# Kernel tuning notes

Measured on AMD Instinct MI355X. Metric: run time of the kernel, lower is better.

The kernel has to match this reference:

```python
import jax, jax.numpy as jnp
import numpy as np

C, H, W = 8, 8, 8
A = 6            # action_dim
LATENT = 64
HID = 64
GRU_IN = HID + A + LATENT  # 134


def _conv(x, w):
    return jax.lax.conv_general_dilated(
        x, w, (1, 1), 'VALID', dimension_numbers=('NCHW', 'OIHW', 'NCHW'))


def setup_inputs() -> dict:
    key = jax.random.key(0)
    ks = jax.random.split(key, 20)
    B, N, T = 64, 10, 128
    s_h = jax.random.normal(ks[0], (B, N, T, C, H, W), jnp.float32)
    a_h = jax.random.randint(ks[1], (B, N, T), 0, A).astype(jnp.int64)
    b_z = jax.random.normal(ks[2], (B, LATENT), jnp.float32)
    s = 0.05
    p = {
        'conv1_w': jax.random.normal(ks[3], (32, C, 3, 3)) * s,
        'conv1_b': jnp.zeros((32,)),
        'conv2_w': jax.random.normal(ks[4], (32, 32, 3, 3)) * s,
        'conv2_b': jnp.zeros((32,)),
        'fc_w': jax.random.normal(ks[5], (HID, 32 * 4 * 4)) * s,
        'fc_b': jnp.zeros((HID,)),
        'emb': jax.random.normal(ks[6], (A, A)) * s,
        'gru_wih': jax.random.normal(ks[7], (3 * HID, GRU_IN)) * s,
        'gru_whh': jax.random.normal(ks[8], (3 * HID, HID)) * s,
        'gru_bih': jnp.zeros((3 * HID,)),
        'gru_bhh': jnp.zeros((3 * HID,)),
        'mlp1_w': jax.random.normal(ks[9], (HID, HID)) * s,
        'mlp1_b': jnp.zeros((HID,)),
        'mlp2_w': jax.random.normal(ks[10], (A, HID)) * s,
        'mlp2_b': jnp.zeros((A,)),
    }
    return {'s_h': s_h, 'a_h': a_h, 'b_z': b_z, **p}


def reference(s_h, a_h, b_z, conv1_w, conv1_b, conv2_w, conv2_b, fc_w, fc_b,
              emb, gru_wih, gru_whh, gru_bih, gru_bhh,
              mlp1_w, mlp1_b, mlp2_w, mlp2_b):
    B, N = s_h.shape[0], s_h.shape[1]
    T = a_h.shape[2]
    BN = B * N

    # action mask, [B, N, T, 1]
    action_masks = (a_h != A - 1)[..., None].astype(jnp.float32)

    # --- state encoder on first frame only ---
    s0 = s_h[:, :, 0].reshape(BN, C, H, W)
    x = jax.nn.relu(_conv(s0, conv1_w) + conv1_b[:, None, None])
    x = jax.nn.relu(_conv(x, conv2_w) + conv2_b[:, None, None])
    x = x.reshape(BN, -1)                       # [BN, 512]
    state_emb = jax.nn.relu(x @ fc_w.T + fc_b)  # [BN, HID]

    bz = jnp.broadcast_to(b_z[:, None, :], (B, N, LATENT)).reshape(BN, LATENT)

    h0 = jnp.zeros((BN, HID), s_h.dtype)
    act0 = jnp.full((BN,), A - 1, jnp.int32)

    def step(carry, _):
        h, act = carry
        a_emb = emb[act]                                          # [BN, A]
        inp = jnp.concatenate([state_emb, a_emb, bz], axis=-1)    # [BN, GRU_IN]
        gx = inp @ gru_wih.T + gru_bih
        gh = h @ gru_whh.T + gru_bhh
        xr, xz, xn = jnp.split(gx, 3, axis=-1)
        hr, hz, hn = jnp.split(gh, 3, axis=-1)
        r = jax.nn.sigmoid(xr + hr)
        z = jax.nn.sigmoid(xz + hz)
        n = jnp.tanh(xn + r * hn)
        h_new = (1.0 - z) * n + z * h
        hid = jnp.tanh(h_new @ mlp1_w.T + mlp1_b)
        logits = hid @ mlp2_w.T + mlp2_b                          # [BN, A]
        next_act = jax.lax.stop_gradient(jnp.argmax(logits, axis=-1)).astype(jnp.int32)
        return (h_new, next_act), logits

    (_, _), logits_seq = jax.lax.scan(step, (h0, act0), None, length=T - 1)
    # logits_seq: [T-1, BN, A] -> [B, N, T-1, A]
    logits_all = jnp.transpose(logits_seq, (1, 0, 2)).reshape(B, N, T - 1, A)
    return logits_all, action_masks
```

## Files before the change

### kernel.cpp

```cpp
#include <hip/hip_runtime.h>

#define A_DIM 6
#define HID_D 64
#define LATENT_D 64
#define GRU_IN_D 134
#define T_STEPS 128
#define N_ENV 10
#define BN_TOT 640

typedef float f2 __attribute__((ext_vector_type(2)));

__device__ __forceinline__ float fast_sigmoid(float x) {
    return __builtin_amdgcn_rcpf(1.0f + __builtin_amdgcn_exp2f(-1.4426950408889634f * x));
}
__device__ __forceinline__ float fast_tanh(float x) {
    return 1.0f - 2.0f * __builtin_amdgcn_rcpf(1.0f + __builtin_amdgcn_exp2f(2.8853900817779268f * x));
}

template<int CTRL>
__device__ __forceinline__ float dppadd(float v) {
    int t = __builtin_amdgcn_update_dpp(0, __builtin_bit_cast(int, v), CTRL, 0xf, 0xf, true);
    return v + __builtin_bit_cast(float, t);
}
__device__ __forceinline__ float wave_reduce_add(float v) {
    v = dppadd<0x111>(v);
    v = dppadd<0x112>(v);
    v = dppadd<0x114>(v);
    v = dppadd<0x118>(v);
    v = dppadd<0x142>(v);
    v = dppadd<0x143>(v);
    return __builtin_bit_cast(float, __builtin_amdgcn_readlane(__builtin_bit_cast(int, v), 63));
}

__global__ __launch_bounds__(128, 1)
void policy_kernel(const float* __restrict__ s_h,
                   const int*   __restrict__ a_h,
                   const float* __restrict__ b_z,
                   const float* __restrict__ conv1_w, const float* __restrict__ conv1_b,
                   const float* __restrict__ conv2_w, const float* __restrict__ conv2_b,
                   const float* __restrict__ fc_w,    const float* __restrict__ fc_b,
                   const float* __restrict__ emb,
                   const float* __restrict__ gru_wih, const float* __restrict__ gru_whh,
                   const float* __restrict__ gru_bih, const float* __restrict__ gru_bhh,
                   const float* __restrict__ mlp1_w,  const float* __restrict__ mlp1_b,
                   const float* __restrict__ mlp2_w,  const float* __restrict__ mlp2_b,
                   float* __restrict__ logits_out, float* __restrict__ mask_out)
{
    __shared__ __align__(16) float s0[512];
    __shared__ __align__(16) float a1[1152];
    __shared__ __align__(16) float a2[512];
    __shared__ __align__(16) float pfc[128];
    __shared__ __align__(16) float semb[64];
    __shared__ __align__(16) float gxc[192];
    __shared__ __align__(16) float atab[6*192];
    __shared__ __align__(16) float hbuf[64];

    const int bn  = blockIdx.x;
    const int tid = threadIdx.x;
    const int j   = tid & 63;
    const int w   = tid >> 6;

    mask_out[bn * T_STEPS + tid] = (a_h[bn * T_STEPS + tid] != (A_DIM - 1)) ? 1.0f : 0.0f;

    {
        const float* src = s_h + (size_t)bn * T_STEPS * 512;
        #pragma unroll
        for (int i = 0; i < 4; ++i) s0[tid + i * 128] = src[tid + i * 128];
    }
    __syncthreads();

    for (int i = tid; i < 1152; i += 128) {
        const int oc = i / 36, r = i % 36, oh = r / 6, ow = r % 6;
        float sum = conv1_b[oc];
        const float* wp = conv1_w + oc * 72;
        #pragma unroll
        for (int ic = 0; ic < 8; ++ic)
            #pragma unroll
            for (int kh = 0; kh < 3; ++kh)
                #pragma unroll
                for (int kw = 0; kw < 3; ++kw)
                    sum = fmaf(s0[ic * 64 + (oh + kh) * 8 + (ow + kw)],
                               wp[ic * 9 + kh * 3 + kw], sum);
        a1[i] = fmaxf(sum, 0.0f);
    }
    __syncthreads();

    for (int i = tid; i < 512; i += 128) {
        const int oc = i / 16, r = i % 16, oh = r / 4, ow = r % 4;
        float sum = conv2_b[oc];
        const float* wp = conv2_w + oc * 288;
        for (int ic = 0; ic < 32; ++ic)
            #pragma unroll
            for (int kh = 0; kh < 3; ++kh)
                #pragma unroll
                for (int kw = 0; kw < 3; ++kw)
                    sum = fmaf(a1[ic * 36 + (oh + kh) * 6 + (ow + kw)],
                               wp[ic * 9 + kh * 3 + kw], sum);
        a2[i] = fmaxf(sum, 0.0f);
    }
    __syncthreads();

    {
        const float* wp = fc_w + j * 512 + w * 256;
        const float* ap = a2 + w * 256;
        float s0a = 0.f, s1a = 0.f, s2a = 0.f, s3a = 0.f;
        for (int k = 0; k < 256; k += 4) {
            s0a = fmaf(ap[k + 0], wp[k + 0], s0a);
            s1a = fmaf(ap[k + 1], wp[k + 1], s1a);
            s2a = fmaf(ap[k + 2], wp[k + 2], s2a);
            s3a = fmaf(ap[k + 3], wp[k + 3], s3a);
        }
        pfc[tid] = (s0a + s1a) + (s2a + s3a);
    }
    __syncthreads();
    if (tid < 64) semb[tid] = fmaxf(pfc[tid] + pfc[tid + 64] + fc_b[tid], 0.0f);
    __syncthreads();

    {
        const float* bz = b_z + (size_t)(bn / N_ENV) * LATENT_D;
        for (int g = tid; g < 192; g += 128) {
            float sum = gru_bih[g] + ((g < 128) ? gru_bhh[g] : 0.0f);
            const float* wp = gru_wih + g * GRU_IN_D;
            for (int k = 0; k < 64; ++k) sum = fmaf(semb[k], wp[k], sum);
            for (int k = 0; k < 64; ++k) sum = fmaf(bz[k], wp[70 + k], sum);
            gxc[g] = sum;
        }
    }
    for (int i = tid; i < 6 * 192; i += 128) {
        const int a = i / 192, g = i % 192;
        float sum = 0.0f;
        #pragma unroll
        for (int q = 0; q < 6; ++q)
            sum = fmaf(emb[a * 6 + q], gru_wih[g * GRU_IN_D + 64 + q], sum);
        atab[i] = sum;
    }
    __syncthreads();

    if (w == 1) return;

    f2 wr[32], wz[32], wn[32], w1[32];
    {
        const float* pr = gru_whh + (size_t)j * 64;
        const float* pz = gru_whh + (size_t)(64 + j) * 64;
        const float* pn = gru_whh + (size_t)(128 + j) * 64;
        const float* p1 = mlp1_w + (size_t)j * 64;
        #pragma unroll
        for (int i = 0; i < 16; ++i) {
            float4 v;
            v = ((const float4*)pr)[i]; wr[2*i] = (f2){v.x, v.y}; wr[2*i+1] = (f2){v.z, v.w};
            v = ((const float4*)pz)[i]; wz[2*i] = (f2){v.x, v.y}; wz[2*i+1] = (f2){v.z, v.w};
            v = ((const float4*)pn)[i]; wn[2*i] = (f2){v.x, v.y}; wn[2*i+1] = (f2){v.z, v.w};
            v = ((const float4*)p1)[i]; w1[2*i] = (f2){v.x, v.y}; w1[2*i+1] = (f2){v.z, v.w};
        }
    }
    const float gxr = gxc[j], gxz = gxc[64 + j], gxn = gxc[128 + j];
    const float bhn = gru_bhh[128 + j];
    const float b1j = mlp1_b[j];
    float ar[6], az[6], an[6], m2c[6], b2[6];
    #pragma unroll
    for (int a = 0; a < 6; ++a) {
        ar[a] = atab[a * 192 + j];
        az[a] = atab[a * 192 + 64 + j];
        an[a] = atab[a * 192 + 128 + j];
        m2c[a] = mlp2_w[a * 64 + j];
        b2[a] = mlp2_b[a];
    }

    float hprev = 0.0f;
    float hr_c = 0.0f, hz_c = 0.0f, hn_c = bhn;
    int act = A_DIM - 1;
    float* lout = logits_out + (size_t)bn * (T_STEPS - 1) * A_DIM;
    const float4* hb = (const float4*)hbuf;

    for (int t = 0; t < T_STEPS - 1; ++t) {
        float sr = ar[0], sz = az[0], sn = an[0];
        #pragma unroll
        for (int a = 1; a < 6; ++a) {
            const bool c = (act == a);
            sr = c ? ar[a] : sr; sz = c ? az[a] : sz; sn = c ? an[a] : sn;
        }
        const float r = fast_sigmoid(gxr + sr + hr_c);
        const float z = fast_sigmoid(gxz + sz + hz_c);
        const float n = fast_tanh(fmaf(r, hn_c, gxn + sn));
        const float hnew = fmaf(z, hprev - n, n);
        hprev = hnew;

        __builtin_amdgcn_wave_barrier();
        hbuf[j] = hnew;
        __builtin_amdgcn_wave_barrier();

        f2 p1 = {0.f, 0.f}, pr = {0.f, 0.f}, pz = {0.f, 0.f}, pn = {0.f, 0.f};
        #pragma unroll
        for (int i = 0; i < 16; ++i) {
            const float4 hv = hb[i];
            const f2 ha = (f2){hv.x, hv.y};
            const f2 hc = (f2){hv.z, hv.w};
            p1 += ha * w1[2*i]; p1 += hc * w1[2*i+1];
            pr += ha * wr[2*i]; pr += hc * wr[2*i+1];
            pz += ha * wz[2*i]; pz += hc * wz[2*i+1];
            pn += ha * wn[2*i]; pn += hc * wn[2*i+1];
        }
        hr_c = pr.x + pr.y;
        hz_c = pz.x + pz.y;
        hn_c = pn.x + pn.y + bhn;
        const float hid = fast_tanh(p1.x + p1.y + b1j);

        const float l0 = wave_reduce_add(hid * m2c[0]) + b2[0];
        const float l1 = wave_reduce_add(hid * m2c[1]) + b2[1];
        const float l2 = wave_reduce_add(hid * m2c[2]) + b2[2];
        const float l3 = wave_reduce_add(hid * m2c[3]) + b2[3];
        const float l4 = wave_reduce_add(hid * m2c[4]) + b2[4];
        const float l5 = wave_reduce_add(hid * m2c[5]) + b2[5];

        float best = l0; int bi = 0;
        if (l1 > best) { best = l1; bi = 1; }
        if (l2 > best) { best = l2; bi = 2; }
        if (l3 > best) { best = l3; bi = 3; }
        if (l4 > best) { best = l4; bi = 4; }
        if (l5 > best) { best = l5; bi = 5; }
        act = bi;

        if (j < A_DIM) {
            const float outv = (j == 0) ? l0 : (j == 1) ? l1 : (j == 2) ? l2
                             : (j == 3) ? l3 : (j == 4) ? l4 : l5;
            lout[t * A_DIM + j] = outv;
        }
    }
}

extern "C" void kernel_launch(void* const* d_in, const int* in_sizes, int n_in,
                              void* d_out, int out_size, void* d_ws, size_t ws_size,
                              hipStream_t stream) {
    const float* s_h     = (const float*)d_in[0];
    const int*   a_h     = (const int*)  d_in[1];
    const float* b_z     = (const float*)d_in[2];
    const float* conv1_w = (const float*)d_in[3];
    const float* conv1_b = (const float*)d_in[4];
    const float* conv2_w = (const float*)d_in[5];
    const float* conv2_b = (const float*)d_in[6];
    const float* fc_w    = (const float*)d_in[7];
    const float* fc_b    = (const float*)d_in[8];
    const float* emb     = (const float*)d_in[9];
    const float* gru_wih = (const float*)d_in[10];
    const float* gru_whh = (const float*)d_in[11];
    const float* gru_bih = (const float*)d_in[12];
    const float* gru_bhh = (const float*)d_in[13];
    const float* mlp1_w  = (const float*)d_in[14];
    const float* mlp1_b  = (const float*)d_in[15];
    const float* mlp2_w  = (const float*)d_in[16];
    const float* mlp2_b  = (const float*)d_in[17];

    float* out = (float*)d_out;
    float* logits_out = out;
    float* mask_out   = out + (size_t)BN_TOT * (T_STEPS - 1) * A_DIM;

    policy_kernel<<<BN_TOT, 128, 0, stream>>>(
        s_h, a_h, b_z, conv1_w, conv1_b, conv2_w, conv2_b, fc_w, fc_b, emb,
        gru_wih, gru_whh, gru_bih, gru_bhh, mlp1_w, mlp1_b, mlp2_w, mlp2_b,
        logits_out, mask_out);
}
```

Baseline: 482.9 us.

## Speculatively compute GRU hidden state for all six actions to shorten the recurrence chain

```diff
diff --git a/kernel.cpp b/kernel.cpp
--- a/kernel.cpp
+++ b/kernel.cpp
@@ -53,7 +53,7 @@
     __shared__ __align__(16) float semb[64];
     __shared__ __align__(16) float gxc[192];
     __shared__ __align__(16) float atab[6*192];
-    __shared__ __align__(16) float hbuf[64];
+    __shared__ __align__(16) float hspec[6*64];
 
     const int bn  = blockIdx.x;
     const int tid = threadIdx.x;
@@ -153,57 +153,60 @@
             v = ((const float4*)p1)[i]; w1[2*i] = (f2){v.x, v.y}; w1[2*i+1] = (f2){v.z, v.w};
         }
     }
-    const float gxr = gxc[j], gxz = gxc[64 + j], gxn = gxc[128 + j];
     const float bhn = gru_bhh[128 + j];
     const float b1j = mlp1_b[j];
-    float ar[6], az[6], an[6], m2c[6], b2[6];
+    float arx[6], azx[6], anx[6], m2c[6], b2[6];
+    {
+        const float gxr = gxc[j], gxz = gxc[64 + j], gxn = gxc[128 + j];
+        #pragma unroll
+        for (int a = 0; a < 6; ++a) {
+            arx[a] = gxr + atab[a * 192 + j];
+            azx[a] = gxz + atab[a * 192 + 64 + j];
+            anx[a] = gxn + atab[a * 192 + 128 + j];
+            m2c[a] = mlp2_w[a * 64 + j];
+            b2[a] = mlp2_b[a];
+        }
+    }
+
+    float ha[6];
     #pragma unroll
     for (int a = 0; a < 6; ++a) {
-        ar[a] = atab[a * 192 + j];
-        az[a] = atab[a * 192 + 64 + j];
-        an[a] = atab[a * 192 + 128 + j];
-        m2c[a] = mlp2_w[a * 64 + j];
-        b2[a] = mlp2_b[a];
-    }
-
-    float hprev = 0.0f;
-    float hr_c = 0.0f, hz_c = 0.0f, hn_c = bhn;
+        const float r = fast_sigmoid(arx[a]);
+        const float z = fast_sigmoid(azx[a]);
+        const float n = fast_tanh(fmaf(r, bhn, anx[a]));
+        ha[a] = fmaf(z, 0.0f - n, n);
+    }
+    __builtin_amdgcn_wave_barrier();
+    #pragma unroll
+    for (int a = 0; a < 6; ++a) hspec[a * 64 + j] = ha[a];
+    __builtin_amdgcn_wave_barrier();
+
     int act = A_DIM - 1;
     float* lout = logits_out + (size_t)bn * (T_STEPS - 1) * A_DIM;
-    const float4* hb = (const float4*)hbuf;
 
     for (int t = 0; t < T_STEPS - 1; ++t) {
-        float sr = ar[0], sz = az[0], sn = an[0];
-        #pragma unroll
-        for (int a = 1; a < 6; ++a) {
-            const bool c = (act == a);
-            sr = c ? ar[a] : sr; sz = c ? az[a] : sz; sn = c ? an[a] : sn;
-        }
-        const float r = fast_sigmoid(gxr + sr + hr_c);
-        const float z = fast_sigmoid(gxz + sz + hz_c);
-        const float n = fast_tanh(fmaf(r, hn_c, gxn + sn));
-        const float hnew = fmaf(z, hprev - n, n);
-        hprev = hnew;
-
-        __builtin_amdgcn_wave_barrier();
-        hbuf[j] = hnew;
-        __builtin_amdgcn_wave_barrier();
-
-        f2 p1 = {0.f, 0.f}, pr = {0.f, 0.f}, pz = {0.f, 0.f}, pn = {0.f, 0.f};
+        const float4* hb = (const float4*)(hspec + (act << 6));
+        float hprev = ha[0];
+        #pragma unroll
+        for (int a = 1; a < 6; ++a) hprev = (act == a) ? ha[a] : hprev;
+
+        f2 p1a = {0.f, 0.f}, p1b = {0.f, 0.f};
+        f2 pr = {0.f, 0.f}, pz = {0.f, 0.f}, pn = {0.f, 0.f};
         #pragma unroll
         for (int i = 0; i < 16; ++i) {
             const float4 hv = hb[i];
-            const f2 ha = (f2){hv.x, hv.y};
-            const f2 hc = (f2){hv.z, hv.w};
-            p1 += ha * w1[2*i]; p1 += hc * w1[2*i+1];
-            pr += ha * wr[2*i]; pr += hc * wr[2*i+1];
-            pz += ha * wz[2*i]; pz += hc * wz[2*i+1];
-            pn += ha * wn[2*i]; pn += hc * wn[2*i+1];
-        }
-        hr_c = pr.x + pr.y;
-        hz_c = pz.x + pz.y;
-        hn_c = pn.x + pn.y + bhn;
+            const f2 haa = (f2){hv.x, hv.y};
+            const f2 hcc = (f2){hv.z, hv.w};
+            p1a += haa * w1[2*i]; p1b += hcc * w1[2*i+1];
+            pr += haa * wr[2*i]; pr += hcc * wr[2*i+1];
+            pz += haa * wz[2*i]; pz += hcc * wz[2*i+1];
+            pn += haa * wn[2*i]; pn += hcc * wn[2*i+1];
+        }
+        const f2 p1 = p1a + p1b;
         const float hid = fast_tanh(p1.x + p1.y + b1j);
+        const float hr = pr.x + pr.y;
+        const float hz = pz.x + pz.y;
+        const float hn = pn.x + pn.y + bhn;
 
         const float l0 = wave_reduce_add(hid * m2c[0]) + b2[0];
         const float l1 = wave_reduce_add(hid * m2c[1]) + b2[1];
@@ -211,6 +214,18 @@
         const float l3 = wave_reduce_add(hid * m2c[3]) + b2[3];
         const float l4 = wave_reduce_add(hid * m2c[4]) + b2[4];
         const float l5 = wave_reduce_add(hid * m2c[5]) + b2[5];
+
+        #pragma unroll
+        for (int a = 0; a < 6; ++a) {
+            const float r = fast_sigmoid(arx[a] + hr);
+            const float z = fast_sigmoid(azx[a] + hz);
+            const float n = fast_tanh(fmaf(r, hn, anx[a]));
+            ha[a] = fmaf(z, hprev - n, n);
+        }
+        __builtin_amdgcn_wave_barrier();
+        #pragma unroll
+        for (int a = 0; a < 6; ++a) hspec[a * 64 + j] = ha[a];
+        __builtin_amdgcn_wave_barrier();
 
         float best = l0; int bi = 0;
         if (l1 > best) { best = l1; bi = 1; }
```

New measurement: 480.9 us. No clear change (-0.4%).
